# Kernel tuning notes

Measured on AMD Instinct MI355X. Metric: run time of the kernel, lower is better.

The kernel has to match this reference:

```python
import jax, jax.numpy as jnp
import numpy as np

B, DIN, D, C, M, NF = 64, 150528, 512, 100, 64, 256
EPS = 1e-6


def setup_inputs() -> dict:
    key = jax.random.key(0)
    ks = jax.random.split(key, 6)
    image = jax.random.normal(ks[0], (B, DIN), jnp.float32) * 0.02
    W_enc = jax.random.normal(ks[1], (DIN, D), jnp.float32) * 0.01
    text = jax.random.normal(ks[2], (C, D), jnp.float32)
    text_features = text / jnp.linalg.norm(text, axis=-1, keepdims=True)
    keys = jax.random.normal(ks[3], (C, M, D), jnp.float32)
    keys_all = keys / jnp.linalg.norm(keys, axis=-1, keepdims=True)
    indices = jax.random.randint(ks[4], (C, NF), 0, D, dtype=jnp.int32)
    return {
        "image": image,
        "W_enc": W_enc,
        "text_features": text_features,
        "keys_all": keys_all,
        "logit_scale": jnp.float32(np.log(100.0)),
        "indices": indices,
        "alpha": jnp.float32(1.0),
        "beta": jnp.float32(5.5),
        "gamma": jnp.float32(0.1),
    }


def reference(image, W_enc, text_features, keys_all, logit_scale, indices, alpha, beta, gamma):
    # image encoder (dense GEMM stand-in for clip_model.visual) + L2 normalize
    f = image @ W_enc                                    # [B, D]
    f = f / jnp.linalg.norm(f, axis=-1, keepdims=True)
    clip_logits = jnp.exp(logit_scale) * (f @ text_features.T)   # [B, C]

    # per-class feature-dim gathers (vectorized over classes)
    keys_sel = jax.vmap(lambda k, idx: k[:, idx])(keys_all, indices)      # [C, M, NF]
    text_sel = jax.vmap(lambda idx: text_features[:, idx])(indices)       # [C, C, NF]  (text_sel[c, j, f])
    img_sel = f[:, indices]                                               # [B, C, NF]

    # cache similarities: per-class [B, M] matmul, scaled by number of keys
    sims = jnp.einsum('bcf,cmf->bcm', img_sel, keys_sel) / M              # [B, C, M]

    # key logits and softmax over classes
    key_logits = jax.nn.softmax(jnp.einsum('cmf,cjf->cmj', keys_sel, text_sel), axis=-1)  # [C, M, C]

    # KL(one_hot(c) || key_logits) in log2; only the j==c term is nonzero
    p_cc = key_logits[jnp.arange(C)[:, None], jnp.arange(M)[None, :], jnp.arange(C)[:, None]]  # [C, M]
    KL = jnp.log2((1.0 + EPS) / (p_cc + EPS))                             # [C, M]
    w = jnp.exp(KL * gamma)                                               # soft_values nonzero entries

    # block-diagonal soft_values => cache_logits[b, c] = sum_m sims[b, c, m] * w[c, m]
    cache = jnp.einsum('bcm,cm->bc', sims, w)                             # [B, C]
    cache_logits = jnp.exp(-(beta - beta * cache))
    return alpha * cache_logits + clip_logits
```

## Files before the change

### kernel.cpp

```cpp
#include <hip/hip_runtime.h>

#define DIN 150528
#define DD 512
#define NC 100
#define NM 64
#define NFEAT 256
#define EPSF 1e-6f
#define KSTEPS (DIN / 32)

typedef float f32x4 __attribute__((ext_vector_type(4)));
typedef __bf16 bf16x8 __attribute__((ext_vector_type(8)));
typedef unsigned short u16x8 __attribute__((ext_vector_type(8)));

static __device__ __forceinline__ unsigned short f2bf(float x) {
  unsigned int u = __builtin_bit_cast(unsigned int, x);
  u += 0x7FFFu + ((u >> 16) & 1u);
  return (unsigned short)(u >> 16);
}
static __device__ __forceinline__ float bf2f(unsigned short h) {
  return __builtin_bit_cast(float, ((unsigned int)h) << 16);
}

__global__ __launch_bounds__(256, 1) void gemm_f(
    const float* __restrict__ image, const float* __restrict__ W,
    float* __restrict__ f_part) {
  const int tid = threadIdx.x;
  const int wv = tid >> 6;
  const int lane = tid & 63;
  const int q = lane >> 4;
  const int r16 = lane & 15;
  const int nb = wv * 128;

  f32x4 acc[4][8];
#pragma unroll
  for (int mt = 0; mt < 4; ++mt)
#pragma unroll
    for (int nt = 0; nt < 8; ++nt)
#pragma unroll
      for (int r = 0; r < 4; ++r) acc[mt][nt][r] = 0.0f;

  const int b = blockIdx.x;
  const int s0 = (b * KSTEPS) >> 8;
  const int s1 = ((b + 1) * KSTEPS) >> 8;

  for (int s = s0; s < s1; ++s) {
    const int k0 = s * 32;
    f32x4 alo[4], ahi[4];
#pragma unroll
    for (int mt = 0; mt < 4; ++mt) {
      const float* ap = image + (size_t)(mt * 16 + r16) * DIN + (k0 + q * 8);
      alo[mt] = *(const f32x4*)ap;
      ahi[mt] = *(const f32x4*)(ap + 4);
    }
    float wr[8][8];
#pragma unroll
    for (int nt = 0; nt < 8; ++nt) {
      const float* wp = W + (size_t)(k0 + q * 8) * DD + (nb + nt * 16 + r16);
#pragma unroll
      for (int j = 0; j < 8; ++j) wr[nt][j] = wp[(size_t)j * DD];
    }
    bf16x8 av[4];
#pragma unroll
    for (int mt = 0; mt < 4; ++mt) {
      u16x8 u;
      u[0] = f2bf(alo[mt][0]); u[1] = f2bf(alo[mt][1]);
      u[2] = f2bf(alo[mt][2]); u[3] = f2bf(alo[mt][3]);
      u[4] = f2bf(ahi[mt][0]); u[5] = f2bf(ahi[mt][1]);
      u[6] = f2bf(ahi[mt][2]); u[7] = f2bf(ahi[mt][3]);
      av[mt] = __builtin_bit_cast(bf16x8, u);
    }
    bf16x8 bv[8];
#pragma unroll
    for (int nt = 0; nt < 8; ++nt) {
      u16x8 u;
#pragma unroll
      for (int j = 0; j < 8; ++j) u[j] = f2bf(wr[nt][j]);
      bv[nt] = __builtin_bit_cast(bf16x8, u);
    }
#pragma unroll
    for (int mt = 0; mt < 4; ++mt)
#pragma unroll
      for (int nt = 0; nt < 8; ++nt)
        acc[mt][nt] = __builtin_amdgcn_mfma_f32_16x16x32_bf16(
            av[mt], bv[nt], acc[mt][nt], 0, 0, 0);
  }

  float* outp = f_part + (size_t)b * (NM * DD);
#pragma unroll
  for (int mt = 0; mt < 4; ++mt)
#pragma unroll
    for (int nt = 0; nt < 8; ++nt) {
      const int n = nb + nt * 16 + r16;
#pragma unroll
      for (int r = 0; r < 4; ++r) {
        const int m = mt * 16 + q * 4 + r;
        outp[m * DD + n] = acc[mt][nt][r];
      }
    }
}

__global__ __launch_bounds__(128) void reduce_f(
    const float* __restrict__ f_part, float* __restrict__ f) {
  const int m = blockIdx.x >> 2;
  const int n = (blockIdx.x & 3) * 128 + threadIdx.x;
  const float* p = f_part + (size_t)m * DD + n;
  float s = 0.0f;
#pragma unroll 16
  for (int sdx = 0; sdx < 256; ++sdx) s += p[(size_t)sdx * (NM * DD)];
  f[m * DD + n] = s;
}

__global__ void norm_f(const float* __restrict__ f, float* __restrict__ fn) {
  const int b = blockIdx.x;
  const int t = threadIdx.x;
  float s = 0.0f;
#pragma unroll
  for (int i = 0; i < 8; ++i) {
    float v = f[b * DD + t + i * 64];
    s += v * v;
  }
#pragma unroll
  for (int o = 32; o; o >>= 1) s += __shfl_xor(s, o);
  const float inv = 1.0f / sqrtf(s);
#pragma unroll
  for (int i = 0; i < 8; ++i)
    fn[b * DD + t + i * 64] = f[b * DD + t + i * 64] * inv;
}

__global__ __launch_bounds__(256) void wk_kernel(
    const float* __restrict__ text, const float* __restrict__ keys,
    const int* __restrict__ indices, const float* __restrict__ pgamma,
    float* __restrict__ kw_buf) {
  const int c = blockIdx.x;
  const int t = threadIdx.x;
  const int wv = t >> 6, lane = t & 63;
  const int q = lane >> 4, r16 = lane & 15;

  __shared__ __align__(16) unsigned short A_lds[64 * 264];
  __shared__ __align__(16) unsigned short B_lds[112 * 136];
  __shared__ __align__(16) int idx_s[256];

  idx_s[t] = indices[c * 256 + t];
  __syncthreads();

  {
    const int j = t;
    const float* kp = keys + (size_t)c * 64 * 512 + idx_s[j];
#pragma unroll 8
    for (int m = 0; m < 64; ++m) A_lds[m * 264 + j] = f2bf(kp[(size_t)m * 512]);
  }

  f32x4 acc[7];
#pragma unroll
  for (int nt = 0; nt < 7; ++nt)
#pragma unroll
    for (int r = 0; r < 4; ++r) acc[nt][r] = 0.0f;
  const int mt = wv;

  for (int kh = 0; kh < 2; ++kh) {
    __syncthreads();
    {
      const int kk = t & 127;
      const float* tp = text + idx_s[kh * 128 + kk];
      for (int n = (t >> 7); n < 112; n += 2)
        B_lds[n * 136 + kk] =
            (n < NC) ? f2bf(tp[(size_t)n * 512]) : (unsigned short)0;
    }
    __syncthreads();
#pragma unroll
    for (int ks = 0; ks < 4; ++ks) {
      bf16x8 afr = *(const bf16x8*)(A_lds + (mt * 16 + r16) * 264 + kh * 128 +
                                    ks * 32 + q * 8);
#pragma unroll
      for (int nt = 0; nt < 7; ++nt) {
        bf16x8 bfr =
            *(const bf16x8*)(B_lds + (nt * 16 + r16) * 136 + ks * 32 + q * 8);
        acc[nt] = __builtin_amdgcn_mfma_f32_16x16x32_bf16(afr, bfr, acc[nt],
                                                          0, 0, 0);
      }
    }
  }
  __syncthreads();

  float* C_lds = reinterpret_cast<float*>(B_lds);
#pragma unroll
  for (int nt = 0; nt < 7; ++nt) {
    const int j2 = nt * 16 + r16;
#pragma unroll
    for (int r = 0; r < 4; ++r) {
      const int m = mt * 16 + q * 4 + r;
      C_lds[m * 113 + j2] = acc[nt][r];
    }
  }
  __syncthreads();

  float* w_lds = reinterpret_cast<float*>(idx_s);
  if (t < 64) {
    const int m = t;
    float mx = -1e30f;
    for (int j2 = 0; j2 < NC; ++j2) mx = fmaxf(mx, C_lds[m * 113 + j2]);
    float sum = 0.0f;
    for (int j2 = 0; j2 < NC; ++j2) sum += expf(C_lds[m * 113 + j2] - mx);
    const float p = expf(C_lds[m * 113 + c] - mx) / sum;
    const float KL = log2f((1.0f + EPSF) / (p + EPSF));
    w_lds[m] = expf(KL * (*pgamma));
  }
  __syncthreads();
  {
    const int j = t;
    float kwv = 0.0f;
#pragma unroll 8
    for (int m = 0; m < 64; ++m) kwv += w_lds[m] * bf2f(A_lds[m * 264 + j]);
    kw_buf[c * 256 + j] = kwv;
  }
}

__global__ __launch_bounds__(256) void final_kernel(
    const float* __restrict__ fn, const float* __restrict__ text,
    const int* __restrict__ indices, const float* __restrict__ kw_buf,
    const float* __restrict__ pls, const float* __restrict__ palpha,
    const float* __restrict__ pbeta, float* __restrict__ out) {
  const int c = blockIdx.x;
  const int wv = threadIdx.x >> 6, lane = threadIdx.x & 63;

  int idx4[4];
  float kw4[4];
#pragma unroll
  for (int i = 0; i < 4; ++i) {
    idx4[i] = indices[c * 256 + i * 64 + lane];
    kw4[i] = kw_buf[c * 256 + i * 64 + lane];
  }
  float tc[8];
#pragma unroll
  for (int i = 0; i < 8; ++i) tc[i] = text[c * 512 + i * 64 + lane];
  const float ls = expf(*pls);
  const float alpha = *palpha, beta = *pbeta;

  for (int b = wv; b < 64; b += 4) {
    const float* fr = fn + b * DD;
    float cp = 0.0f, lp = 0.0f;
#pragma unroll
    for (int i = 0; i < 4; ++i) cp += fr[idx4[i]] * kw4[i];
#pragma unroll
    for (int i = 0; i < 8; ++i) lp += fr[i * 64 + lane] * tc[i];
#pragma unroll
    for (int o = 32; o; o >>= 1) {
      cp += __shfl_xor(cp, o);
      lp += __shfl_xor(lp, o);
    }
    if (lane == 0)
      out[b * NC + c] =
          alpha * expf(beta * (cp * (1.0f / 64.0f)) - beta) + ls * lp;
  }
}

extern "C" void kernel_launch(void* const* d_in, const int* in_sizes, int n_in,
                              void* d_out, int out_size, void* d_ws,
                              size_t ws_size, hipStream_t stream) {
  const float* image = (const float*)d_in[0];
  const float* W = (const float*)d_in[1];
  const float* text = (const float*)d_in[2];
  const float* keys = (const float*)d_in[3];
  const float* pls = (const float*)d_in[4];
  const int* idx = (const int*)d_in[5];
  const float* palpha = (const float*)d_in[6];
  const float* pbeta = (const float*)d_in[7];
  const float* pgamma = (const float*)d_in[8];
  float* out = (float*)d_out;

  char* ws = (char*)d_ws;
  float* f_part = (float*)(ws);
  float* f_buf = (float*)(ws + 33554432);
  float* fn = (float*)(ws + 33554432 + 131072);
  float* kw = (float*)(ws + 33554432 + 262144);

  gemm_f<<<256, 256, 0, stream>>>(image, W, f_part);
  reduce_f<<<256, 128, 0, stream>>>(f_part, f_buf);
  norm_f<<<64, 64, 0, stream>>>(f_buf, fn);
  wk_kernel<<<NC, 256, 0, stream>>>(text, keys, idx, pgamma, kw);
  final_kernel<<<NC, 256, 0, stream>>>(fn, text, idx, kw, pls, palpha, pbeta,
                                       out);
}
```

Baseline: 524.1 us.

## Double-buffer W tiles into LDS via async global_load_lds in GEMM

The split-K GEMM now loads each 32x512 fp32 W tile into a double-buffered LDS array with direct global-to-LDS loads, prefetching the next step while the current one computes. B fragments are then read from LDS instead of strided per-lane global loads, and a block barrier is added each step. It also raises the unroll factor in the partial-sum reduction. This uses 128KB of LDS and adds a barrier per step, and the fp32 LDS reads with stride DD may cause bank conflicts.

```diff
diff --git a/kernel.cpp b/kernel.cpp
--- a/kernel.cpp
+++ b/kernel.cpp
@@ -31,6 +31,8 @@
   const int r16 = lane & 15;
   const int nb = wv * 128;
 
+  __shared__ __align__(16) float Wlds[2][32 * DD];
+
   f32x4 acc[4][8];
 #pragma unroll
   for (int mt = 0; mt < 4; ++mt)
@@ -43,6 +45,24 @@
   const int s0 = (b * KSTEPS) >> 8;
   const int s1 = ((b + 1) * KSTEPS) >> 8;
 
+  auto stage = [&](int s, int buf) {
+    const char* gsrc = (const char*)(W + (size_t)s * 32 * DD);
+    char* lbase = (char*)(&Wlds[buf][0]);
+    const int woff = wv << 14;
+#pragma unroll
+    for (int i = 0; i < 16; ++i) {
+      const int off = woff + (i << 10);
+      __builtin_amdgcn_global_load_lds(
+          (const __attribute__((address_space(1))) void*)(gsrc + off +
+                                                          (lane << 4)),
+          (__attribute__((address_space(3))) void*)(lbase + off), 16, 0, 0);
+    }
+  };
+
+  stage(s0, 0);
+  __syncthreads();
+
+  int cur = 0;
   for (int s = s0; s < s1; ++s) {
     const int k0 = s * 32;
     f32x4 alo[4], ahi[4];
@@ -52,13 +72,8 @@
       alo[mt] = *(const f32x4*)ap;
       ahi[mt] = *(const f32x4*)(ap + 4);
     }
-    float wr[8][8];
-#pragma unroll
-    for (int nt = 0; nt < 8; ++nt) {
-      const float* wp = W + (size_t)(k0 + q * 8) * DD + (nb + nt * 16 + r16);
-#pragma unroll
-      for (int j = 0; j < 8; ++j) wr[nt][j] = wp[(size_t)j * DD];
-    }
+    if (s + 1 < s1) stage(s + 1, cur ^ 1);
+
     bf16x8 av[4];
 #pragma unroll
     for (int mt = 0; mt < 4; ++mt) {
@@ -69,20 +84,22 @@
       u[6] = f2bf(ahi[mt][2]); u[7] = f2bf(ahi[mt][3]);
       av[mt] = __builtin_bit_cast(bf16x8, u);
     }
-    bf16x8 bv[8];
+    const float* wb = &Wlds[cur][0];
 #pragma unroll
     for (int nt = 0; nt < 8; ++nt) {
       u16x8 u;
 #pragma unroll
-      for (int j = 0; j < 8; ++j) u[j] = f2bf(wr[nt][j]);
-      bv[nt] = __builtin_bit_cast(bf16x8, u);
-    }
-#pragma unroll
-    for (int mt = 0; mt < 4; ++mt)
-#pragma unroll
-      for (int nt = 0; nt < 8; ++nt)
+      for (int j = 0; j < 8; ++j)
+        u[j] = f2bf(wb[(q * 8 + j) * DD + nb + nt * 16 + r16]);
+      const bf16x8 bvv = __builtin_bit_cast(bf16x8, u);
+#pragma unroll
+      for (int mt = 0; mt < 4; ++mt)
         acc[mt][nt] = __builtin_amdgcn_mfma_f32_16x16x32_bf16(
-            av[mt], bv[nt], acc[mt][nt], 0, 0, 0);
+            av[mt], bvv, acc[mt][nt], 0, 0, 0);
+    }
+
+    __syncthreads();
+    cur ^= 1;
   }
 
   float* outp = f_part + (size_t)b * (NM * DD);
@@ -105,7 +122,7 @@
   const int n = (blockIdx.x & 3) * 128 + threadIdx.x;
   const float* p = f_part + (size_t)m * DD + n;
   float s = 0.0f;
-#pragma unroll 16
+#pragma unroll 32
   for (int sdx = 0; sdx < 256; ++sdx) s += p[(size_t)sdx * (NM * DD)];
   f[m * DD + n] = s;
 }
```

Measured after the change: 518.2 us. Within noise of the previous version (-1.1%).
